# Kernel optimization log

Hardware: AMD Instinct MI355X
Metric: run time of the kernel (lower is better)

Reference implementation:

```python
import jax, jax.numpy as jnp
import numpy as np

D_MODEL = 1024
NUM_HEADS = 16
D_K = D_MODEL // NUM_HEADS


def setup_inputs() -> dict:
    key = jax.random.key(0)
    ks = jax.random.split(key, 11)
    B, S = 2, 2048
    scale = 1.0 / np.sqrt(D_MODEL)
    inp = {
        'q': jax.random.normal(ks[0], (B, S, D_MODEL), dtype=jnp.float32),
        'k': jax.random.normal(ks[1], (B, S, D_MODEL), dtype=jnp.float32),
        'v': jax.random.normal(ks[2], (B, S, D_MODEL), dtype=jnp.float32),
        'W_q': jax.random.normal(ks[3], (D_MODEL, D_MODEL), dtype=jnp.float32) * scale,
        'b_q': jnp.zeros((D_MODEL,), dtype=jnp.float32),
        'W_k': jax.random.normal(ks[4], (D_MODEL, D_MODEL), dtype=jnp.float32) * scale,
        'b_k': jnp.zeros((D_MODEL,), dtype=jnp.float32),
        'W_v': jax.random.normal(ks[5], (D_MODEL, D_MODEL), dtype=jnp.float32) * scale,
        'b_v': jnp.zeros((D_MODEL,), dtype=jnp.float32),
        'W_o': jax.random.normal(ks[6], (D_MODEL, D_MODEL), dtype=jnp.float32) * scale,
        'b_o': jnp.zeros((D_MODEL,), dtype=jnp.float32),
    }
    return inp


def _split_heads(x):
    # [B, S, D] -> [B, H, S, d_k]
    B, S, _ = x.shape
    return x.reshape(B, S, NUM_HEADS, D_K).transpose(0, 2, 1, 3)


def reference(q, k, v, W_q, b_q, W_k, b_k, W_v, b_v, W_o, b_o):
    # Linear projections (torch Linear: x @ W.T + b)
    qh = _split_heads(q @ W_q.T + b_q)  # [B,H,S,dk]
    kh = _split_heads(k @ W_k.T + b_k)
    vh = _split_heads(v @ W_v.T + b_v)
    scores = jnp.einsum('bhsd,bhtd->bhst', qh, kh) / jnp.sqrt(
        jnp.asarray(D_K, dtype=qh.dtype))  # [B,H,S,S]
    probs = jax.nn.softmax(scores, axis=-1)
    attn = jnp.einsum('bhst,bhtd->bhsd', probs, vh)  # [B,H,S,dk]
    B, H, S, dk = attn.shape
    combined = attn.transpose(0, 2, 1, 3).reshape(B, S, H * dk)  # [B,S,D]
    return combined @ W_o.T + b_o
```

## Files before the change

kernel.cpp:

```cpp
#include <hip/hip_runtime.h>
#include <hip/hip_bf16.h>

typedef __bf16 bf16;
typedef __attribute__((ext_vector_type(4))) __bf16 bf16x4;
typedef __attribute__((ext_vector_type(8))) __bf16 bf16x8;
typedef __attribute__((ext_vector_type(4))) float f32x4;
typedef __attribute__((ext_vector_type(4))) short short4v;

#define AS1C(p) ((const __attribute__((address_space(1))) void*)(p))
#define AS3(p)  ((__attribute__((address_space(3))) void*)(p))

static constexpr int B_ = 2, S_ = 2048, DM = 1024, H_ = 16, DK = 64;
static constexpr int M_ = B_ * S_;
static constexpr int NW = DM * DM;
static constexpr float QSCL = 0.125f * 1.44269504088896340736f;

__device__ __forceinline__ float fast_exp2(float x) {
#if __has_builtin(__builtin_amdgcn_exp2f)
  return __builtin_amdgcn_exp2f(x);
#else
  return exp2f(x);
#endif
}

__device__ __forceinline__ f32x4 mfma_pv(bf16x4 a, bf16x4 b, f32x4 c) {
#if __has_builtin(__builtin_amdgcn_mfma_f32_16x16x16_bf16)
  return __builtin_amdgcn_mfma_f32_16x16x16_bf16(a, b, c, 0, 0, 0);
#else
  union U { bf16x4 h; short4v s; };
  U ua; ua.h = a;
  U ub; ub.h = b;
  return __builtin_amdgcn_mfma_f32_16x16x16bf16_1k(ua.s, ub.s, c, 0, 0, 0);
#endif
}

__global__ __launch_bounds__(256) void cast_w4(
    const float* Wq, const float* Wk, const float* Wv, const float* Wo,
    bf16* Wc, bf16* WoC)
{
  const int z = blockIdx.y;
  const float* in = z == 0 ? Wq : (z == 1 ? Wk : (z == 2 ? Wv : Wo));
  const float s = z == 0 ? QSCL : 1.0f;
  bf16* out = z < 3 ? (Wc + (size_t)z * NW) : WoC;
  const int i = (blockIdx.x * 256 + threadIdx.x) * 8;
  f32x4 a = *(const f32x4*)(in + i);
  f32x4 b = *(const f32x4*)(in + i + 4);
  bf16x8 o;
#pragma unroll
  for (int j = 0; j < 4; ++j) { o[j] = (bf16)(a[j] * s); o[4 + j] = (bf16)(b[j] * s); }
  *(bf16x8*)(out + i) = o;
}

template<int WTM, bool A_BF16, bool OUT_F32>
__device__ __forceinline__ void gemm_body(
    const void* __restrict__ Ain, const bf16* __restrict__ W,
    const float* __restrict__ bias, float bscale, void* __restrict__ Cout,
    bool transv, int M, int N, int K, int bx, int by)
{
  constexpr int BMt = 2 * WTM;
  constexpr int WI  = WTM / 16;
  __shared__ bf16 As[2 * BMt * 32];
  __shared__ bf16 Bs[2 * 128 * 32];

  const int tid  = threadIdx.x;
  const int wave = tid >> 6, lane = tid & 63;
  const int quad = lane >> 4, l16 = lane & 15;
  const int wm = wave >> 1, wn = wave & 1;
  const int row0 = by * BMt;
  const int col0 = bx * 128;

  const int srow  = lane >> 2;
  const int skcol = (lane & 3) * 8;

  const int arow  = (tid >> 1) & (BMt - 1);
  const int ak16  = (tid & 1) * 16;
  const float* agp = nullptr;
  f32x4 pre[8];
  if constexpr (!A_BF16) {
    agp = (const float*)Ain + (size_t)(row0 + arow) * K + ak16;
#pragma unroll
    for (int hf = 0; hf < 2; ++hf)
#pragma unroll
      for (int c = 0; c < 4; ++c)
        pre[hf * 4 + c] = *(const f32x4*)(agp + hf * 32 + c * 4);
  }

  f32x4 acc[WI][4] = {};

  for (int k0 = 0; k0 < K; k0 += 64) {
    __syncthreads();
    if constexpr (A_BF16) {
      const bf16* A = (const bf16*)Ain;
#pragma unroll
      for (int hf = 0; hf < 2; ++hf)
#pragma unroll
        for (int c = wave; c < BMt / 16; c += 4)
          __builtin_amdgcn_global_load_lds(
              AS1C(A + (size_t)(row0 + c * 16 + srow) * K + k0 + hf * 32 + skcol),
              AS3(As + hf * BMt * 32 + c * 16 * 32), 16, 0, 0);
    } else {
#pragma unroll
      for (int hf = 0; hf < 2; ++hf) {
        bf16x8 w0, w1;
#pragma unroll
        for (int j = 0; j < 4; ++j) {
          w0[j]     = (bf16)pre[hf * 4 + 0][j];
          w0[4 + j] = (bf16)pre[hf * 4 + 1][j];
          w1[j]     = (bf16)pre[hf * 4 + 2][j];
          w1[4 + j] = (bf16)pre[hf * 4 + 3][j];
        }
        bf16* dst = As + hf * BMt * 32 + arow * 32 + ak16;
        *(bf16x8*)dst = w0;
        *(bf16x8*)(dst + 8) = w1;
      }
    }
#pragma unroll
    for (int hf = 0; hf < 2; ++hf)
#pragma unroll
      for (int i = 0; i < 2; ++i) {
        const int c = wave * 2 + i;
        __builtin_amdgcn_global_load_lds(
            AS1C(W + (size_t)(col0 + c * 16 + srow) * K + k0 + hf * 32 + skcol),
            AS3(Bs + hf * 128 * 32 + c * 16 * 32), 16, 0, 0);
      }
    __syncthreads();

    if constexpr (!A_BF16) {
      if (k0 + 64 < K) {
#pragma unroll
        for (int hf = 0; hf < 2; ++hf)
#pragma unroll
          for (int c = 0; c < 4; ++c)
            pre[hf * 4 + c] = *(const f32x4*)(agp + k0 + 64 + hf * 32 + c * 4);
      }
    }

#pragma unroll
    for (int hf = 0; hf < 2; ++hf) {
      bf16x8 a[WI], bfr[4];
#pragma unroll
      for (int i = 0; i < WI; ++i)
        a[i] = *(const bf16x8*)(As + hf * BMt * 32 + (wm * WTM + i * 16 + l16) * 32 + quad * 8);
#pragma unroll
      for (int j = 0; j < 4; ++j)
        bfr[j] = *(const bf16x8*)(Bs + hf * 128 * 32 + (wn * 64 + j * 16 + l16) * 32 + quad * 8);
#pragma unroll
      for (int i = 0; i < WI; ++i)
#pragma unroll
        for (int j = 0; j < 4; ++j)
          acc[i][j] = __builtin_amdgcn_mfma_f32_16x16x32_bf16(a[i], bfr[j], acc[i][j], 0, 0, 0);
    }
  }

#pragma unroll
  for (int j = 0; j < 4; ++j) {
    const int col = col0 + wn * 64 + j * 16 + l16;
    const float bv = bias[col] * bscale;
    if (!OUT_F32 && transv) {
      const int hh = col >> 6, dd = col & 63;
#pragma unroll
      for (int i = 0; i < WI; ++i) {
        const int row = row0 + wm * WTM + i * 16 + quad * 4;
        const int bb2 = row >> 11, tok = row & 2047;
        bf16x4 o;
#pragma unroll
        for (int r = 0; r < 4; ++r) o[r] = (bf16)(acc[i][j][r] + bv);
        *(bf16x4*)((bf16*)Cout + (((size_t)bb2 * H_ + hh) * DK + dd) * S_ + tok) = o;
      }
    } else {
#pragma unroll
      for (int i = 0; i < WI; ++i) {
#pragma unroll
        for (int r = 0; r < 4; ++r) {
          const int row = row0 + wm * WTM + i * 16 + quad * 4 + r;
          const float val = acc[i][j][r] + bv;
          if constexpr (OUT_F32)
            ((float*)Cout)[(size_t)row * N + col] = val;
          else
            ((bf16*)Cout)[(size_t)row * N + col] = (bf16)val;
        }
      }
    }
  }
}

__global__ __launch_bounds__(256) void gemm_qkv(
    const float* A0, const float* A1, const float* A2,
    const bf16* __restrict__ Wc,
    const float* b0, const float* b1, const float* b2,
    bf16* C0, bf16* C1, bf16* C2, int M, int N, int K)
{
  const int id = blockIdx.x;
  const int z  = id >> 8;
  const int r  = id & 255;
  const int by = r & 31;
  const int bx = r >> 5;
  const float* A = z == 0 ? A0 : (z == 1 ? A1 : A2);
  const float* bias = z == 0 ? b0 : (z == 1 ? b1 : b2);
  const float bscale = z == 0 ? QSCL : 1.0f;
  bf16* C = z == 0 ? C0 : (z == 1 ? C1 : C2);
  gemm_body<64, false, false>(A, Wc + (size_t)z * NW, bias, bscale, C,
                              z == 2, M, N, K, bx, by);
}

__global__ __launch_bounds__(256) void gemm_out(
    const bf16* __restrict__ Ain, const bf16* __restrict__ W,
    const float* __restrict__ bias, float* __restrict__ Cout,
    int M, int N, int K)
{
  const int id = blockIdx.x;
  const int by = id & 63;
  const int bx = id >> 6;
  gemm_body<32, true, true>(Ain, W, bias, 1.0f, Cout, false, M, N, K, bx, by);
}

__global__ __launch_bounds__(256, 2) void attn_kernel(
    const bf16* Q, const bf16* __restrict__ Kb,
    const bf16* __restrict__ Vtg, bf16* O)
{
  __shared__ bf16 Kt[2 * 64 * 64];
  __shared__ bf16 Vt[2 * 64 * 64];

  const int tid  = threadIdx.x;
  const int wave = tid >> 6, lane = tid & 63;
  const int quad = lane >> 4, l16 = lane & 15;
  const int id = blockIdx.x;
  const int hb = id & 31;
  const int h = hb & 15, b = hb >> 4;
  const int qt = id >> 5;
  const int qA = qt * 128 + wave * 32;
  const size_t base  = (size_t)b * S_ * DM + (size_t)h * DK;
  const size_t baseV = ((size_t)b * H_ + h) * DK * S_;

  bf16x8 qf[2][2];
#pragma unroll
  for (int f = 0; f < 2; ++f)
#pragma unroll
    for (int kt = 0; kt < 2; ++kt)
      qf[f][kt] = *(const bf16x8*)(Q + base + (size_t)(qA + f * 16 + l16) * DM + kt * 32 + quad * 8);

  const bool kside = (wave < 2);
  const int srow  = kside ? (tid >> 1) : ((tid - 128) >> 1);
  const int shalf = tid & 1;
  const bf16* gp = kside
      ? (Kb + base + (size_t)srow * DM + shalf * 32)
      : (Vtg + baseV + (size_t)srow * S_ + shalf * 32);
  const size_t gstep = kside ? (size_t)64 * DM : 64;
  char* sb = (char*)(kside ? (void*)Kt : (void*)Vt) + srow * 128;
  const int sw_s = (srow & 7) << 4;

  bf16x8 st[4];
#pragma unroll
  for (int c = 0; c < 4; ++c) st[c] = *(const bf16x8*)(gp + c * 8);
  gp += gstep;
#pragma unroll
  for (int c = 0; c < 4; ++c)
    *(bf16x8*)(sb + ((shalf * 64 + c * 16) ^ sw_s)) = st[c];
#pragma unroll
  for (int c = 0; c < 4; ++c) st[c] = *(const bf16x8*)(gp + c * 8);
  gp += gstep;

  f32x4 lacc[2] = {};
  f32x4 accO[2][4] = {};
  const int sw = (l16 & 7) << 4;

  __syncthreads();

  constexpr int NIT = S_ / 64;
  for (int it = 0; it < NIT; ++it) {
    const int cur = it & 1, nxt = cur ^ 1;
    const char* Kc = (const char*)Kt + cur * 8192;
    const char* Vc = (const char*)Vt + cur * 8192;

    f32x4 sc[2][4];
#pragma unroll
    for (int ct = 0; ct < 4; ++ct) {
      const char* kp = Kc + (ct * 16 + l16) * 128;
      const bf16x8 kf0 = *(const bf16x8*)(kp + ((quad * 16) ^ sw));
      const bf16x8 kf1 = *(const bf16x8*)(kp + ((64 + quad * 16) ^ sw));
#pragma unroll
      for (int f = 0; f < 2; ++f) {
        f32x4 a = {0.f, 0.f, 0.f, 0.f};
        a = __builtin_amdgcn_mfma_f32_16x16x32_bf16(kf0, qf[f][0], a, 0, 0, 0);
        a = __builtin_amdgcn_mfma_f32_16x16x32_bf16(kf1, qf[f][1], a, 0, 0, 0);
        sc[f][ct] = a;
      }
    }

    if (it + 1 < NIT) {
#pragma unroll
      for (int c = 0; c < 4; ++c)
        *(bf16x8*)(sb + nxt * 8192 + ((shalf * 64 + c * 16) ^ sw_s)) = st[c];
      if (it + 2 < NIT) {
#pragma unroll
        for (int c = 0; c < 4; ++c) st[c] = *(const bf16x8*)(gp + c * 8);
        gp += gstep;
      }
    }

    bf16x4 pk[2][4];
#pragma unroll
    for (int f = 0; f < 2; ++f)
#pragma unroll
      for (int ct = 0; ct < 4; ++ct)
#pragma unroll
        for (int r = 0; r < 4; ++r) {
          const float p = fast_exp2(sc[f][ct][r]);
          lacc[f][r] += p;
          pk[f][ct][r] = (bf16)p;
        }

#pragma unroll
    for (int dt = 0; dt < 4; ++dt) {
      const char* vp = Vc + (dt * 16 + l16) * 128;
#pragma unroll
      for (int ct = 0; ct < 4; ++ct) {
        const bf16x4 vf = *(const bf16x4*)(vp + ((ct * 32 + quad * 8) ^ sw));
#pragma unroll
        for (int f = 0; f < 2; ++f)
          accO[f][dt] = mfma_pv(vf, pk[f][ct], accO[f][dt]);
      }
    }

    __syncthreads();
  }

#pragma unroll
  for (int f = 0; f < 2; ++f) {
    float l_s = (lacc[f][0] + lacc[f][1]) + (lacc[f][2] + lacc[f][3]);
    l_s += __shfl_xor(l_s, 16, 64);
    l_s += __shfl_xor(l_s, 32, 64);
    const float inv = 1.0f / l_s;
#pragma unroll
    for (int dt = 0; dt < 4; ++dt) {
      bf16x4 o;
#pragma unroll
      for (int r = 0; r < 4; ++r) o[r] = (bf16)(accO[f][dt][r] * inv);
      *(bf16x4*)(O + base + (size_t)(qA + f * 16 + l16) * DM + dt * 16 + quad * 4) = o;
    }
  }
}

extern "C" void kernel_launch(void* const* d_in, const int* in_sizes, int n_in,
                              void* d_out, int out_size, void* d_ws, size_t ws_size,
                              hipStream_t stream) {
  (void)in_sizes; (void)n_in; (void)out_size; (void)ws_size;
  const float* q  = (const float*)d_in[0];
  const float* k  = (const float*)d_in[1];
  const float* v  = (const float*)d_in[2];
  const float* Wq = (const float*)d_in[3];
  const float* bq = (const float*)d_in[4];
  const float* Wk = (const float*)d_in[5];
  const float* bk = (const float*)d_in[6];
  const float* Wv = (const float*)d_in[7];
  const float* bvv= (const float*)d_in[8];
  const float* Wo = (const float*)d_in[9];
  const float* bo = (const float*)d_in[10];
  float* out = (float*)d_out;

  char* ws = (char*)d_ws;
  const size_t MB = 1024 * 1024;
  bf16* Qb  = (bf16*)(ws);
  bf16* Kbf = (bf16*)(ws + 8 * MB);
  bf16* Vtg = (bf16*)(ws + 16 * MB);
  bf16* Wc  = (bf16*)(ws + 24 * MB);
  bf16* WoC = (bf16*)(ws + 30 * MB);
  bf16* Ab  = Qb;

  dim3 bb(256, 1, 1);

  cast_w4<<<dim3(NW / 2048, 4, 1), bb, 0, stream>>>(Wq, Wk, Wv, Wo, Wc, WoC);

  gemm_qkv<<<dim3(768, 1, 1), bb, 0, stream>>>(
      q, k, v, Wc, bq, bk, bvv, Qb, Kbf, Vtg, M_, DM, DM);

  attn_kernel<<<dim3(512, 1, 1), bb, 0, stream>>>(Qb, Kbf, Vtg, Ab);

  gemm_out<<<dim3(512, 1, 1), bb, 0, stream>>>(Ab, WoC, bo, out, M_, DM, DM);
}
```

Measured before the change: 216.8 us.

## Double-buffer GEMM shared-memory tiles to overlap global loads with MFMA

Restructures the shared GEMM body so the W tile (and the bf16 A tile in the output projection) is double-buffered in LDS. The next k-slice's async global-to-LDS loads are issued before computing on the current buffer, with one barrier per iteration. The fp32 A path keeps its register prefetch with a single A buffer. Launch-bound occupancy hints are also added, which trades larger LDS use and possible register pressure against hidden load latency.

```diff
diff --git a/kernel.cpp b/kernel.cpp
--- a/kernel.cpp
+++ b/kernel.cpp
@@ -59,8 +59,9 @@
 {
   constexpr int BMt = 2 * WTM;
   constexpr int WI  = WTM / 16;
-  __shared__ bf16 As[2 * BMt * 32];
-  __shared__ bf16 Bs[2 * 128 * 32];
+  constexpr int ABUF = A_BF16 ? 2 : 1;
+  __shared__ bf16 As[ABUF * BMt * 64];
+  __shared__ bf16 Bs[2 * 128 * 64];
 
   const int tid  = threadIdx.x;
   const int wave = tid >> 6, lane = tid & 63;
@@ -72,33 +73,56 @@
   const int srow  = lane >> 2;
   const int skcol = (lane & 3) * 8;
 
+  const bf16*  Abf = (const bf16*)Ain;
+  const float* Afp = (const float*)Ain;
+
+  auto stage_W = [&](int k0, int buf) {
+#pragma unroll
+    for (int hf = 0; hf < 2; ++hf)
+#pragma unroll
+      for (int i = 0; i < 2; ++i) {
+        const int c = wave * 2 + i;
+        __builtin_amdgcn_global_load_lds(
+            AS1C(W + (size_t)(col0 + c * 16 + srow) * K + k0 + hf * 32 + skcol),
+            AS3(Bs + buf * (128 * 64) + hf * 128 * 32 + c * 16 * 32), 16, 0, 0);
+      }
+  };
+  auto stage_Abf = [&](int k0, int buf) {
+#pragma unroll
+    for (int hf = 0; hf < 2; ++hf)
+#pragma unroll
+      for (int c = wave; c < BMt / 16; c += 4)
+        __builtin_amdgcn_global_load_lds(
+            AS1C(Abf + (size_t)(row0 + c * 16 + srow) * K + k0 + hf * 32 + skcol),
+            AS3(As + buf * (BMt * 64) + hf * BMt * 32 + c * 16 * 32), 16, 0, 0);
+  };
+
   const int arow  = (tid >> 1) & (BMt - 1);
   const int ak16  = (tid & 1) * 16;
   const float* agp = nullptr;
   f32x4 pre[8];
+
   if constexpr (!A_BF16) {
-    agp = (const float*)Ain + (size_t)(row0 + arow) * K + ak16;
+    agp = Afp + (size_t)(row0 + arow) * K + ak16;
 #pragma unroll
     for (int hf = 0; hf < 2; ++hf)
 #pragma unroll
       for (int c = 0; c < 4; ++c)
         pre[hf * 4 + c] = *(const f32x4*)(agp + hf * 32 + c * 4);
+    stage_W(0, 0);
+  } else {
+    stage_Abf(0, 0);
+    stage_W(0, 0);
+    __syncthreads();
   }
 
   f32x4 acc[WI][4] = {};
 
-  for (int k0 = 0; k0 < K; k0 += 64) {
-    __syncthreads();
-    if constexpr (A_BF16) {
-      const bf16* A = (const bf16*)Ain;
-#pragma unroll
-      for (int hf = 0; hf < 2; ++hf)
-#pragma unroll
-        for (int c = wave; c < BMt / 16; c += 4)
-          __builtin_amdgcn_global_load_lds(
-              AS1C(A + (size_t)(row0 + c * 16 + srow) * K + k0 + hf * 32 + skcol),
-              AS3(As + hf * BMt * 32 + c * 16 * 32), 16, 0, 0);
-    } else {
+  const int NK = K / 64;
+  for (int t = 0; t < NK; ++t) {
+    const int cur = t & 1, nxt = cur ^ 1;
+
+    if constexpr (!A_BF16) {
 #pragma unroll
       for (int hf = 0; hf < 2; ++hf) {
         bf16x8 w0, w1;
@@ -113,43 +137,41 @@
         *(bf16x8*)dst = w0;
         *(bf16x8*)(dst + 8) = w1;
       }
-    }
-#pragma unroll
-    for (int hf = 0; hf < 2; ++hf)
-#pragma unroll
-      for (int i = 0; i < 2; ++i) {
-        const int c = wave * 2 + i;
-        __builtin_amdgcn_global_load_lds(
-            AS1C(W + (size_t)(col0 + c * 16 + srow) * K + k0 + hf * 32 + skcol),
-            AS3(Bs + hf * 128 * 32 + c * 16 * 32), 16, 0, 0);
-      }
-    __syncthreads();
-
-    if constexpr (!A_BF16) {
-      if (k0 + 64 < K) {
+      __syncthreads();
+      if (t + 1 < NK) {
+        stage_W((t + 1) * 64, nxt);
 #pragma unroll
         for (int hf = 0; hf < 2; ++hf)
 #pragma unroll
           for (int c = 0; c < 4; ++c)
-            pre[hf * 4 + c] = *(const f32x4*)(agp + k0 + 64 + hf * 32 + c * 4);
-      }
-    }
-
+            pre[hf * 4 + c] = *(const f32x4*)(agp + (t + 1) * 64 + hf * 32 + c * 4);
+      }
+    } else {
+      if (t + 1 < NK) {
+        stage_Abf((t + 1) * 64, nxt);
+        stage_W((t + 1) * 64, nxt);
+      }
+    }
+
+    const bf16* Ab = As + (A_BF16 ? cur * (BMt * 64) : 0);
+    const bf16* Bb = Bs + cur * (128 * 64);
 #pragma unroll
     for (int hf = 0; hf < 2; ++hf) {
       bf16x8 a[WI], bfr[4];
 #pragma unroll
       for (int i = 0; i < WI; ++i)
-        a[i] = *(const bf16x8*)(As + hf * BMt * 32 + (wm * WTM + i * 16 + l16) * 32 + quad * 8);
+        a[i] = *(const bf16x8*)(Ab + hf * BMt * 32 + (wm * WTM + i * 16 + l16) * 32 + quad * 8);
 #pragma unroll
       for (int j = 0; j < 4; ++j)
-        bfr[j] = *(const bf16x8*)(Bs + hf * 128 * 32 + (wn * 64 + j * 16 + l16) * 32 + quad * 8);
+        bfr[j] = *(const bf16x8*)(Bb + hf * 128 * 32 + (wn * 64 + j * 16 + l16) * 32 + quad * 8);
 #pragma unroll
       for (int i = 0; i < WI; ++i)
 #pragma unroll
         for (int j = 0; j < 4; ++j)
           acc[i][j] = __builtin_amdgcn_mfma_f32_16x16x32_bf16(a[i], bfr[j], acc[i][j], 0, 0, 0);
     }
+
+    if (t + 1 < NK) __syncthreads();
   }
 
 #pragma unroll
@@ -184,7 +206,7 @@
   }
 }
 
-__global__ __launch_bounds__(256) void gemm_qkv(
+__global__ __launch_bounds__(256, 3) void gemm_qkv(
     const float* A0, const float* A1, const float* A2,
     const bf16* __restrict__ Wc,
     const float* b0, const float* b1, const float* b2,
@@ -203,7 +225,7 @@
                               z == 2, M, N, K, bx, by);
 }
 
-__global__ __launch_bounds__(256) void gemm_out(
+__global__ __launch_bounds__(256, 2) void gemm_out(
     const bf16* __restrict__ Ain, const bf16* __restrict__ W,
     const float* __restrict__ bias, float* __restrict__ Cout,
     int M, int N, int K)
```

After: 219.4 us. About the same (+1.2%).
